# Kernel tuning notes

Measured on AMD Instinct MI355X. Metric: run time of the kernel, lower is better.

## Reference

```python
import jax, jax.numpy as jnp
import numpy as np

N_NODES = 50000
N_EDGES = 800000
IN_CH, OUT_CH, HEADS = 64, 32, 4
NEG_SLOPE = 0.2
BN_EPS = 1e-5


def setup_inputs() -> dict:
    key = jax.random.key(0)
    ks = jax.random.split(key, 9)
    x = jax.random.normal(ks[0], (N_NODES, IN_CH), dtype=jnp.float32)
    pos = jax.random.uniform(ks[1], (N_NODES, 3), dtype=jnp.float32)
    edge_index = jax.random.randint(ks[2], (2, N_EDGES), 0, N_NODES, dtype=jnp.int64)
    s = 1.0 / np.sqrt(IN_CH)
    W_l = jax.random.normal(ks[3], (IN_CH, HEADS * OUT_CH), dtype=jnp.float32) * s
    W_r = jax.random.normal(ks[4], (IN_CH, HEADS * OUT_CH), dtype=jnp.float32) * s
    W_edge = jax.random.normal(ks[5], (3, HEADS * OUT_CH), dtype=jnp.float32) * 0.5
    att = jax.random.normal(ks[6], (HEADS, OUT_CH), dtype=jnp.float32) * (1.0 / np.sqrt(OUT_CH))
    bn_gamma = jax.random.uniform(ks[7], (HEADS * OUT_CH,), dtype=jnp.float32, minval=0.5, maxval=1.5)
    bn_beta = jax.random.normal(ks[8], (HEADS * OUT_CH,), dtype=jnp.float32) * 0.1
    return {"x": x, "pos": pos, "edge_index": edge_index, "W_l": W_l, "W_r": W_r,
            "W_edge": W_edge, "att": att, "bn_gamma": bn_gamma, "bn_beta": bn_beta}


def reference(x, pos, edge_index, W_l, W_r, W_edge, att, bn_gamma, bn_beta):
    N = x.shape[0]
    H, C = att.shape
    # source->target projections (GATv2: lin_l for source/messages, lin_r for target)
    xl = (x @ W_l).reshape(N, H, C)
    xr = (x @ W_r).reshape(N, H, C)
    src, dst = edge_index[0], edge_index[1]
    edge_attr = pos[src] - pos[dst]  # [E,3] relative position as edge feature
    # add self-loops with fill_value='mean' (PyG default)
    loop = jnp.arange(N)
    src = jnp.concatenate([src, loop])
    dst = jnp.concatenate([dst, loop])
    mean_attr = edge_attr.mean(axis=0, keepdims=True)  # [1,3]
    edge_attr = jnp.concatenate([edge_attr, jnp.broadcast_to(mean_attr, (N, 3))], axis=0)
    # per-edge GATv2 score: att . LeakyReLU(x_l[j] + x_r[i] + W_e e_ij)
    e_feat = (edge_attr @ W_edge).reshape(-1, H, C)
    msg = xl[src]                              # [Et,H,C] (reused for aggregation)
    e = msg + xr[dst] + e_feat
    e = jax.nn.leaky_relu(e, NEG_SLOPE)
    score = jnp.einsum('ehc,hc->eh', e, att)   # [Et,H]
    # segment softmax over destination node
    m = jax.ops.segment_max(score, dst, num_segments=N)
    score = jnp.exp(score - m[dst])
    denom = jax.ops.segment_sum(score, dst, num_segments=N)
    alpha = score / (denom[dst] + 1e-16)       # [Et,H]
    out = jax.ops.segment_sum(alpha[:, :, None] * msg, dst, num_segments=N)
    out = out.reshape(N, H * C)
    # BatchNorm over node dimension (training-mode batch statistics, PyG BatchNorm)
    mu = out.mean(axis=0)
    var = out.var(axis=0)
    return (out - mu) / jnp.sqrt(var + BN_EPS) * bn_gamma + bn_beta
```

## Files before the change

### kernel.cpp

```cpp
#include <hip/hip_runtime.h>
#include <hip/hip_bf16.h>

#define N_NODES 50000
#define IN_CH 64
#define HC 128
#define CAP 64
#define NEG_SLOPE 0.2f
#define BN_EPS 1e-5f


__global__ __launch_bounds__(256) void k_gemm(const float* __restrict__ x,
                                              const float* __restrict__ Wl,
                                              const float* __restrict__ Wr,
                                              unsigned int* __restrict__ xl_bf,
                                              float* __restrict__ xr_out,
                                              int* __restrict__ deg,
                                              float* __restrict__ mean_sums,
                                              float* __restrict__ bn_sums,
                                              int* __restrict__ flag,
                                              const int* __restrict__ eidx) {
  {
    int gtid = blockIdx.x * 256 + threadIdx.x;
    if (gtid < N_NODES) deg[gtid] = 1;
    if (gtid < 256) bn_sums[gtid] = 0.f;
    if (gtid < 3) mean_sums[gtid] = 0.f;
    if (blockIdx.x == 0 && threadIdx.x < 64) {
      int w = eidx[2 * threadIdx.x + 1];
      unsigned long long nz = __ballot(w != 0);
      if (threadIdx.x == 0) flag[0] = (nz == 0ULL) ? 1 : 0;
    }
  }

  __shared__ float xs[16][IN_CH];
  __shared__ __hip_bfloat162 wsm[IN_CH][128];
  const int t = threadIdx.x;
  const int row0 = blockIdx.x * 16;

  for (int i = 0; i < 32; ++i) {
    int k = i * 2 + (t >> 7);
    int p = t & 127;
    int cc = p * 2;
    float2 wv;
    if (cc < 128) wv = *(const float2*)(Wl + k * 128 + cc);
    else          wv = *(const float2*)(Wr + k * 128 + (cc - 128));
    wsm[k][p] = __float22bfloat162_rn(wv);
  }
  {
    int r = t >> 4, c4 = (t & 15) * 4;
    *(float4*)&xs[r][c4] = *(const float4*)(x + (row0 + r) * IN_CH + c4);
  }
  __syncthreads();

  const int ct = t & 63;
  const int rt = t >> 6;
  const int c4 = ct * 4;
  const int r4 = rt * 4;

  float acc[4][4];
  #pragma unroll
  for (int a = 0; a < 4; ++a)
    #pragma unroll
    for (int b = 0; b < 4; ++b) acc[a][b] = 0.f;

  #pragma unroll 8
  for (int k = 0; k < IN_CH; ++k) {
    uint2 wraw = *(const uint2*)&wsm[k][ct * 2];
    float2 f01 = __bfloat1622float2(*(__hip_bfloat162*)&wraw.x);
    float2 f23 = __bfloat1622float2(*(__hip_bfloat162*)&wraw.y);
    float wv[4] = {f01.x, f01.y, f23.x, f23.y};
    float xv[4] = {xs[r4][k], xs[r4 + 1][k], xs[r4 + 2][k], xs[r4 + 3][k]};
    #pragma unroll
    for (int a = 0; a < 4; ++a)
      #pragma unroll
      for (int b = 0; b < 4; ++b) acc[a][b] = fmaf(xv[a], wv[b], acc[a][b]);
  }

  #pragma unroll
  for (int a = 0; a < 4; ++a) {
    int row = row0 + r4 + a;
    if (c4 < 128) {
      __hip_bfloat162 b01 = __float22bfloat162_rn(make_float2(acc[a][0], acc[a][1]));
      __hip_bfloat162 b23 = __float22bfloat162_rn(make_float2(acc[a][2], acc[a][3]));
      uint2 u;
      u.x = *(unsigned int*)&b01;
      u.y = *(unsigned int*)&b23;
      *(uint2*)(xl_bf + row * 64 + (c4 >> 1)) = u;
    } else {
      float4 v = make_float4(acc[a][0], acc[a][1], acc[a][2], acc[a][3]);
      *(float4*)(xr_out + row * HC + (c4 - 128)) = v;
    }
  }
}

__global__ __launch_bounds__(256) void k_edges(const int* __restrict__ eidx,
                                               const float* __restrict__ pos,
                                               int* __restrict__ deg,
                                               int* __restrict__ srcs,
                                               float* __restrict__ mean_sums,
                                               const int* __restrict__ flag,
                                               int E) {
  const bool w64 = flag[0] != 0;
  const int tid = blockIdx.x * 256 + threadIdx.x;
  const int base = tid * 8;
  float sx = 0.f, sy = 0.f, sz = 0.f;

  const bool vec_ok = w64 ? ((E & 1) == 0) : ((E & 3) == 0);

  if (base + 8 <= E && vec_ok) {
    int s[8], d[8];
    if (w64) {
      const int4* ps = (const int4*)(eidx + 2 * base);
      int4 A = ps[0], B = ps[1], C = ps[2], D = ps[3];
      s[0]=A.x; s[1]=A.z; s[2]=B.x; s[3]=B.z; s[4]=C.x; s[5]=C.z; s[6]=D.x; s[7]=D.z;
      const int4* pd = (const int4*)(eidx + 2 * E + 2 * base);
      A = pd[0]; B = pd[1]; C = pd[2]; D = pd[3];
      d[0]=A.x; d[1]=A.z; d[2]=B.x; d[3]=B.z; d[4]=C.x; d[5]=C.z; d[6]=D.x; d[7]=D.z;
    } else {
      int4 A = *(const int4*)(eidx + base);
      int4 B = *(const int4*)(eidx + base + 4);
      s[0]=A.x; s[1]=A.y; s[2]=A.z; s[3]=A.w; s[4]=B.x; s[5]=B.y; s[6]=B.z; s[7]=B.w;
      A = *(const int4*)(eidx + E + base);
      B = *(const int4*)(eidx + E + base + 4);
      d[0]=A.x; d[1]=A.y; d[2]=A.z; d[3]=A.w; d[4]=B.x; d[5]=B.y; d[6]=B.z; d[7]=B.w;
    }
    int slot[8];
    #pragma unroll
    for (int k = 0; k < 8; ++k) slot[k] = atomicAdd(&deg[d[k]], 1);
    #pragma unroll
    for (int k = 0; k < 8; ++k)
      if (slot[k] < CAP) srcs[d[k] * CAP + slot[k]] = s[k];
    #pragma unroll
    for (int k = 0; k < 8; ++k) {
      sx += pos[3 * s[k]]     - pos[3 * d[k]];
      sy += pos[3 * s[k] + 1] - pos[3 * d[k] + 1];
      sz += pos[3 * s[k] + 2] - pos[3 * d[k] + 2];
    }
  } else if (base < E) {
    int hi = min(base + 8, E);
    for (int e = base; e < hi; ++e) {
      int s, d;
      if (w64) { s = eidx[2 * e]; d = eidx[2 * (E + e)]; }
      else     { s = eidx[e];     d = eidx[E + e]; }
      int o = atomicAdd(&deg[d], 1);
      if (o < CAP) srcs[d * CAP + o] = s;
      sx += pos[3 * s]     - pos[3 * d];
      sy += pos[3 * s + 1] - pos[3 * d + 1];
      sz += pos[3 * s + 2] - pos[3 * d + 2];
    }
  }

  #pragma unroll
  for (int m = 1; m < 64; m <<= 1) {
    sx += __shfl_xor(sx, m); sy += __shfl_xor(sy, m); sz += __shfl_xor(sz, m);
  }
  __shared__ float red[4][3];
  int wave = threadIdx.x >> 6, lane = threadIdx.x & 63;
  if (lane == 0) { red[wave][0] = sx; red[wave][1] = sy; red[wave][2] = sz; }
  __syncthreads();
  if (threadIdx.x == 0) {
    float a = 0.f, b = 0.f, c = 0.f;
    for (int w = 0; w < 4; ++w) { a += red[w][0]; b += red[w][1]; c += red[w][2]; }
    unsafeAtomicAdd(&mean_sums[0], a);
    unsafeAtomicAdd(&mean_sums[1], b);
    unsafeAtomicAdd(&mean_sums[2], c);
  }
}

__device__ __forceinline__ void edge4(int s, float dx, float dy, float dz, bool valid,
                                      const unsigned int* __restrict__ xl_bf, int l5,
                                      float4 xr4, float4 at4, float4 w0, float4 w1, float4 w2,
                                      float& a0, float& a1, float& a2, float& a3, float& den) {
  uint2 raw = *(const uint2*)(xl_bf + (s << 6) + (l5 << 1));
  float2 x01 = __bfloat1622float2(*(__hip_bfloat162*)&raw.x);
  float2 x23 = __bfloat1622float2(*(__hip_bfloat162*)&raw.y);
  float t0 = x01.x + xr4.x; t0 = fmaf(dx, w0.x, t0); t0 = fmaf(dy, w1.x, t0); t0 = fmaf(dz, w2.x, t0);
  float t1 = x01.y + xr4.y; t1 = fmaf(dx, w0.y, t1); t1 = fmaf(dy, w1.y, t1); t1 = fmaf(dz, w2.y, t1);
  float t2 = x23.x + xr4.z; t2 = fmaf(dx, w0.z, t2); t2 = fmaf(dy, w1.z, t2); t2 = fmaf(dz, w2.z, t2);
  float t3 = x23.y + xr4.w; t3 = fmaf(dx, w0.w, t3); t3 = fmaf(dy, w1.w, t3); t3 = fmaf(dz, w2.w, t3);
  float l0 = fmaf(NEG_SLOPE, fminf(t0, 0.f), fmaxf(t0, 0.f));
  float l1 = fmaf(NEG_SLOPE, fminf(t1, 0.f), fmaxf(t1, 0.f));
  float l2 = fmaf(NEG_SLOPE, fminf(t2, 0.f), fmaxf(t2, 0.f));
  float l3 = fmaf(NEG_SLOPE, fminf(t3, 0.f), fmaxf(t3, 0.f));
  float sc = l0 * at4.x;
  sc = fmaf(l1, at4.y, sc); sc = fmaf(l2, at4.z, sc); sc = fmaf(l3, at4.w, sc);
  sc += __shfl_xor(sc, 1); sc += __shfl_xor(sc, 2); sc += __shfl_xor(sc, 4);
  float e = __expf(sc);
  float p = valid ? e : 0.f;
  den += p;
  a0 = fmaf(p, x01.x, a0); a1 = fmaf(p, x01.y, a1);
  a2 = fmaf(p, x23.x, a2); a3 = fmaf(p, x23.y, a3);
}

__global__ __launch_bounds__(256) void k_agg(const unsigned int* __restrict__ xl_bf,
                                             float* __restrict__ xr_out,
                                             const float* __restrict__ pos,
                                             const float* __restrict__ att,
                                             const float* __restrict__ We,
                                             const float* __restrict__ mean_sums,
                                             const int* __restrict__ srcs,
                                             const int* __restrict__ deg,
                                             float invE) {
  const int lane = threadIdx.x & 63;
  const int half = lane >> 5;
  const int l5 = lane & 31;
  const int c = l5 << 2;

  const float4 at4 = *(const float4*)(att + c);
  const float4 w0 = *(const float4*)(We + c);
  const float4 w1 = *(const float4*)(We + 128 + c);
  const float4 w2 = *(const float4*)(We + 256 + c);
  const float m0 = mean_sums[0] * invE;
  const float m1 = mean_sums[1] * invE;
  const float m2 = mean_sums[2] * invE;

  const int gw = blockIdx.x * 4 + (threadIdx.x >> 6);
  const int W = gridDim.x * 4;

  for (int i = gw; i < N_NODES; i += W) {
    const float4 xr4 = *(const float4*)(xr_out + i * HC + c);
    const float px = pos[3 * i], py = pos[3 * i + 1], pz = pos[3 * i + 2];
    const int di = min(deg[i], CAP);
    const int sreg = srcs[i * CAP + lane];
    float a0 = 0.f, a1 = 0.f, a2 = 0.f, a3 = 0.f, den = 0.f;

    {
      int sA = __shfl(sreg, 1);
      if (half == 0) sA = i;
      bool vA = half < di;
      if (!vA) sA = i;
      int jB = 2 + half;
      int sB = __shfl(sreg, jB);
      bool vB = jB < di;
      if (!vB) sB = i;
      float pax = pos[3 * sA], pay = pos[3 * sA + 1], paz = pos[3 * sA + 2];
      float pbx = pos[3 * sB], pby = pos[3 * sB + 1], pbz = pos[3 * sB + 2];
      float dxA = (half == 0) ? m0 : pax - px;
      float dyA = (half == 0) ? m1 : pay - py;
      float dzA = (half == 0) ? m2 : paz - pz;
      edge4(sA, dxA, dyA, dzA, vA, xl_bf, l5, xr4, at4, w0, w1, w2, a0, a1, a2, a3, den);
      edge4(sB, pbx - px, pby - py, pbz - pz, vB, xl_bf, l5, xr4, at4, w0, w1, w2, a0, a1, a2, a3, den);
    }

    for (int j = 4; j < di; j += 4) {
      int jA = j + half;
      int jB = j + 2 + half;
      int sA = __shfl(sreg, jA);
      int sB = __shfl(sreg, jB);
      bool vA = jA < di;
      bool vB = jB < di;
      if (!vA) sA = i;
      if (!vB) sB = i;
      float pax = pos[3 * sA], pay = pos[3 * sA + 1], paz = pos[3 * sA + 2];
      float pbx = pos[3 * sB], pby = pos[3 * sB + 1], pbz = pos[3 * sB + 2];
      edge4(sA, pax - px, pay - py, paz - pz, vA, xl_bf, l5, xr4, at4, w0, w1, w2, a0, a1, a2, a3, den);
      edge4(sB, pbx - px, pby - py, pbz - pz, vB, xl_bf, l5, xr4, at4, w0, w1, w2, a0, a1, a2, a3, den);
    }

    den += __shfl_xor(den, 32);
    a0 += __shfl_xor(a0, 32);
    a1 += __shfl_xor(a1, 32);
    a2 += __shfl_xor(a2, 32);
    a3 += __shfl_xor(a3, 32);

    float inv = 1.f / (den + 1e-16f);
    if (half == 0) {
      float4 o = make_float4(a0 * inv, a1 * inv, a2 * inv, a3 * inv);
      *(float4*)(xr_out + i * HC + c) = o;
    }
  }
}

__global__ __launch_bounds__(128) void k_bnstats(const float* __restrict__ out,
                                                 float* __restrict__ bn_sums) {
  int c = threadIdx.x;
  float s = 0.f, ss = 0.f;
  int r = blockIdx.x;
  const int g = gridDim.x;
  for (; r + g < N_NODES; r += 2 * g) {
    float v0 = out[r * HC + c];
    float v1 = out[(r + g) * HC + c];
    s += v0; ss = fmaf(v0, v0, ss);
    s += v1; ss = fmaf(v1, v1, ss);
  }
  if (r < N_NODES) {
    float v = out[r * HC + c];
    s += v; ss = fmaf(v, v, ss);
  }
  unsafeAtomicAdd(&bn_sums[c], s);
  unsafeAtomicAdd(&bn_sums[128 + c], ss);
}

__global__ __launch_bounds__(256) void k_bnapply(float* __restrict__ out,
                                                 const float* __restrict__ bn_sums,
                                                 const float* __restrict__ gamma,
                                                 const float* __restrict__ beta,
                                                 int n4) {
  const int stride = gridDim.x * blockDim.x;
  const float invN = 1.f / (float)N_NODES;
  for (int i = blockIdx.x * blockDim.x + threadIdx.x; i < n4; i += stride) {
    int c = (i & 31) * 4;
    float4 v = ((float4*)out)[i];
    float4 s = *(const float4*)(bn_sums + c);
    float4 q = *(const float4*)(bn_sums + 128 + c);
    float4 g = *(const float4*)(gamma + c);
    float4 b = *(const float4*)(beta + c);
    float mu, var, rstd;
    mu = s.x * invN; var = q.x * invN - mu * mu; rstd = rsqrtf(var + BN_EPS);
    v.x = (v.x - mu) * rstd * g.x + b.x;
    mu = s.y * invN; var = q.y * invN - mu * mu; rstd = rsqrtf(var + BN_EPS);
    v.y = (v.y - mu) * rstd * g.y + b.y;
    mu = s.z * invN; var = q.z * invN - mu * mu; rstd = rsqrtf(var + BN_EPS);
    v.z = (v.z - mu) * rstd * g.z + b.z;
    mu = s.w * invN; var = q.w * invN - mu * mu; rstd = rsqrtf(var + BN_EPS);
    v.w = (v.w - mu) * rstd * g.w + b.w;
    ((float4*)out)[i] = v;
  }
}

extern "C" void kernel_launch(void* const* d_in, const int* in_sizes, int n_in,
                              void* d_out, int out_size, void* d_ws, size_t ws_size,
                              hipStream_t stream) {
  const float* x     = (const float*)d_in[0];
  const float* pos   = (const float*)d_in[1];
  const int*   eidx  = (const int*)d_in[2];
  const float* Wl    = (const float*)d_in[3];
  const float* Wr    = (const float*)d_in[4];
  const float* We    = (const float*)d_in[5];
  const float* att   = (const float*)d_in[6];
  const float* gamma = (const float*)d_in[7];
  const float* beta  = (const float*)d_in[8];
  float* out = (float*)d_out;
  const int E = in_sizes[2] / 2;

  char* ws = (char*)d_ws;
  int*   flag      = (int*)(ws + 0);
  float* mean_sums = (float*)(ws + 64);
  float* bn_sums   = (float*)(ws + 1024);
  int*   deg       = (int*)(ws + 4096);
  int*   srcs      = (int*)(ws + (1 << 19));
  unsigned int* xl_bf = (unsigned int*)(ws + (1 << 24));

  k_gemm<<<N_NODES / 16, 256, 0, stream>>>(x, Wl, Wr, xl_bf, out,
                                           deg, mean_sums, bn_sums, flag, eidx);
  int eblocks = (E + 2047) / 2048;
  k_edges<<<eblocks, 256, 0, stream>>>(eidx, pos, deg, srcs, mean_sums, flag, E);
  k_agg<<<2048, 256, 0, stream>>>(xl_bf, out, pos, att, We, mean_sums, srcs, deg,
                                  1.f / (float)E);
  k_bnstats<<<512, 128, 0, stream>>>(out, bn_sums);
  k_bnapply<<<512, 256, 0, stream>>>(out, bn_sums, gamma, beta, out_size / 4);
}
```

Measured before the change: 258.4 us.

## Pack fp16 edge offsets into buckets and fuse BN statistics into aggregation

The edge pass now computes relative positions once and stores them as fp16 together with a 16-bit source index in an 8-byte bucket slot. This removes the per-edge random position gathers in aggregation. BatchNorm sum and sum-of-squares are accumulated inside the aggregation kernel, with a block reduction and atomics, which removes the separate stats kernel and its pass over the output. Costs are a larger bucket write, fp16 precision on edge offsets, and source ids limited to 16 bits.

Result: faster. 251.5 us (-2.7%).

```diff
diff --git a/kernel.cpp b/kernel.cpp
--- a/kernel.cpp
+++ b/kernel.cpp
@@ -1,5 +1,6 @@
 #include <hip/hip_runtime.h>
 #include <hip/hip_bf16.h>
+#include <hip/hip_fp16.h>
 
 #define N_NODES 50000
 #define IN_CH 64
@@ -92,10 +93,18 @@
   }
 }
 
+__device__ __forceinline__ uint2 packslot(int s, float dx, float dy, float dz) {
+  __half2 hxy = __halves2half2(__float2half_rn(dx), __float2half_rn(dy));
+  uint2 r;
+  r.x = *(unsigned int*)&hxy;
+  r.y = ((unsigned int)s << 16) | (unsigned int)__half_as_ushort(__float2half_rn(dz));
+  return r;
+}
+
 __global__ __launch_bounds__(256) void k_edges(const int* __restrict__ eidx,
                                                const float* __restrict__ pos,
                                                int* __restrict__ deg,
-                                               int* __restrict__ srcs,
+                                               uint2* __restrict__ bucket,
                                                float* __restrict__ mean_sums,
                                                const int* __restrict__ flag,
                                                int E) {
@@ -126,15 +135,17 @@
     int slot[8];
     #pragma unroll
     for (int k = 0; k < 8; ++k) slot[k] = atomicAdd(&deg[d[k]], 1);
+    float dx[8], dy[8], dz[8];
+    #pragma unroll
+    for (int k = 0; k < 8; ++k) {
+      dx[k] = pos[3 * s[k]]     - pos[3 * d[k]];
+      dy[k] = pos[3 * s[k] + 1] - pos[3 * d[k] + 1];
+      dz[k] = pos[3 * s[k] + 2] - pos[3 * d[k] + 2];
+      sx += dx[k]; sy += dy[k]; sz += dz[k];
+    }
     #pragma unroll
     for (int k = 0; k < 8; ++k)
-      if (slot[k] < CAP) srcs[d[k] * CAP + slot[k]] = s[k];
-    #pragma unroll
-    for (int k = 0; k < 8; ++k) {
-      sx += pos[3 * s[k]]     - pos[3 * d[k]];
-      sy += pos[3 * s[k] + 1] - pos[3 * d[k] + 1];
-      sz += pos[3 * s[k] + 2] - pos[3 * d[k] + 2];
-    }
+      if (slot[k] < CAP) bucket[d[k] * CAP + slot[k]] = packslot(s[k], dx[k], dy[k], dz[k]);
   } else if (base < E) {
     int hi = min(base + 8, E);
     for (int e = base; e < hi; ++e) {
@@ -142,10 +153,11 @@
       if (w64) { s = eidx[2 * e]; d = eidx[2 * (E + e)]; }
       else     { s = eidx[e];     d = eidx[E + e]; }
       int o = atomicAdd(&deg[d], 1);
-      if (o < CAP) srcs[d * CAP + o] = s;
-      sx += pos[3 * s]     - pos[3 * d];
-      sy += pos[3 * s + 1] - pos[3 * d + 1];
-      sz += pos[3 * s + 2] - pos[3 * d + 2];
+      float dx = pos[3 * s]     - pos[3 * d];
+      float dy = pos[3 * s + 1] - pos[3 * d + 1];
+      float dz = pos[3 * s + 2] - pos[3 * d + 2];
+      sx += dx; sy += dy; sz += dz;
+      if (o < CAP) bucket[d * CAP + o] = packslot(s, dx, dy, dz);
     }
   }
 
@@ -177,10 +189,10 @@
   float t1 = x01.y + xr4.y; t1 = fmaf(dx, w0.y, t1); t1 = fmaf(dy, w1.y, t1); t1 = fmaf(dz, w2.y, t1);
   float t2 = x23.x + xr4.z; t2 = fmaf(dx, w0.z, t2); t2 = fmaf(dy, w1.z, t2); t2 = fmaf(dz, w2.z, t2);
   float t3 = x23.y + xr4.w; t3 = fmaf(dx, w0.w, t3); t3 = fmaf(dy, w1.w, t3); t3 = fmaf(dz, w2.w, t3);
-  float l0 = fmaf(NEG_SLOPE, fminf(t0, 0.f), fmaxf(t0, 0.f));
-  float l1 = fmaf(NEG_SLOPE, fminf(t1, 0.f), fmaxf(t1, 0.f));
-  float l2 = fmaf(NEG_SLOPE, fminf(t2, 0.f), fmaxf(t2, 0.f));
-  float l3 = fmaf(NEG_SLOPE, fminf(t3, 0.f), fmaxf(t3, 0.f));
+  float l0 = fmaxf(t0, NEG_SLOPE * t0);
+  float l1 = fmaxf(t1, NEG_SLOPE * t1);
+  float l2 = fmaxf(t2, NEG_SLOPE * t2);
+  float l3 = fmaxf(t3, NEG_SLOPE * t3);
   float sc = l0 * at4.x;
   sc = fmaf(l1, at4.y, sc); sc = fmaf(l2, at4.z, sc); sc = fmaf(l3, at4.w, sc);
   sc += __shfl_xor(sc, 1); sc += __shfl_xor(sc, 2); sc += __shfl_xor(sc, 4);
@@ -193,17 +205,20 @@
 
 __global__ __launch_bounds__(256) void k_agg(const unsigned int* __restrict__ xl_bf,
                                              float* __restrict__ xr_out,
-                                             const float* __restrict__ pos,
                                              const float* __restrict__ att,
                                              const float* __restrict__ We,
                                              const float* __restrict__ mean_sums,
-                                             const int* __restrict__ srcs,
+                                             const uint2* __restrict__ bucket,
                                              const int* __restrict__ deg,
-                                             float invE) {
+                                             float invE,
+                                             float* __restrict__ bn_sums) {
+  __shared__ __align__(16) float redS[4][128];
+  __shared__ __align__(16) float redQ[4][128];
   const int lane = threadIdx.x & 63;
   const int half = lane >> 5;
   const int l5 = lane & 31;
   const int c = l5 << 2;
+  const int wave = threadIdx.x >> 6;
 
   const float4 at4 = *(const float4*)(att + c);
   const float4 w0 = *(const float4*)(We + c);
@@ -213,47 +228,57 @@
   const float m1 = mean_sums[1] * invE;
   const float m2 = mean_sums[2] * invE;
 
-  const int gw = blockIdx.x * 4 + (threadIdx.x >> 6);
+  const int gw = blockIdx.x * 4 + wave;
   const int W = gridDim.x * 4;
+
+  float4 bs = make_float4(0.f, 0.f, 0.f, 0.f);
+  float4 bq = make_float4(0.f, 0.f, 0.f, 0.f);
 
   for (int i = gw; i < N_NODES; i += W) {
     const float4 xr4 = *(const float4*)(xr_out + i * HC + c);
-    const float px = pos[3 * i], py = pos[3 * i + 1], pz = pos[3 * i + 2];
     const int di = min(deg[i], CAP);
-    const int sreg = srcs[i * CAP + lane];
+    uint2 se = make_uint2(0u, 0u);
+    if (lane < di) se = bucket[i * CAP + lane];
     float a0 = 0.f, a1 = 0.f, a2 = 0.f, a3 = 0.f, den = 0.f;
 
     {
-      int sA = __shfl(sreg, 1);
-      if (half == 0) sA = i;
-      bool vA = half < di;
+      const int jB = 2 + half;
+      uint2 wA, wB;
+      wA.x = (unsigned)__shfl((int)se.x, 1);  wA.y = (unsigned)__shfl((int)se.y, 1);
+      wB.x = (unsigned)__shfl((int)se.x, jB); wB.y = (unsigned)__shfl((int)se.y, jB);
+      float2 dA = __half22float2(*(__half2*)&wA.x);
+      float dzA = __half2float(__ushort_as_half((unsigned short)(wA.y & 0xffffu)));
+      int sA = (int)(wA.y >> 16);
+      if (half == 0) { sA = i; dA.x = m0; dA.y = m1; dzA = m2; }
+      const bool vA = half < di;
       if (!vA) sA = i;
-      int jB = 2 + half;
-      int sB = __shfl(sreg, jB);
-      bool vB = jB < di;
+      float2 dB = __half22float2(*(__half2*)&wB.x);
+      float dzB = __half2float(__ushort_as_half((unsigned short)(wB.y & 0xffffu)));
+      int sB = (int)(wB.y >> 16);
+      const bool vB = jB < di;
       if (!vB) sB = i;
-      float pax = pos[3 * sA], pay = pos[3 * sA + 1], paz = pos[3 * sA + 2];
-      float pbx = pos[3 * sB], pby = pos[3 * sB + 1], pbz = pos[3 * sB + 2];
-      float dxA = (half == 0) ? m0 : pax - px;
-      float dyA = (half == 0) ? m1 : pay - py;
-      float dzA = (half == 0) ? m2 : paz - pz;
-      edge4(sA, dxA, dyA, dzA, vA, xl_bf, l5, xr4, at4, w0, w1, w2, a0, a1, a2, a3, den);
-      edge4(sB, pbx - px, pby - py, pbz - pz, vB, xl_bf, l5, xr4, at4, w0, w1, w2, a0, a1, a2, a3, den);
+      edge4(sA, dA.x, dA.y, dzA, vA, xl_bf, l5, xr4, at4, w0, w1, w2, a0, a1, a2, a3, den);
+      edge4(sB, dB.x, dB.y, dzB, vB, xl_bf, l5, xr4, at4, w0, w1, w2, a0, a1, a2, a3, den);
     }
 
     for (int j = 4; j < di; j += 4) {
-      int jA = j + half;
-      int jB = j + 2 + half;
-      int sA = __shfl(sreg, jA);
-      int sB = __shfl(sreg, jB);
-      bool vA = jA < di;
-      bool vB = jB < di;
+      const int jA = j + half;
+      const int jB = j + 2 + half;
+      uint2 wA, wB;
+      wA.x = (unsigned)__shfl((int)se.x, jA); wA.y = (unsigned)__shfl((int)se.y, jA);
+      wB.x = (unsigned)__shfl((int)se.x, jB); wB.y = (unsigned)__shfl((int)se.y, jB);
+      float2 dA = __half22float2(*(__half2*)&wA.x);
+      float dzA = __half2float(__ushort_as_half((unsigned short)(wA.y & 0xffffu)));
+      int sA = (int)(wA.y >> 16);
+      const bool vA = jA < di;
       if (!vA) sA = i;
+      float2 dB = __half22float2(*(__half2*)&wB.x);
+      float dzB = __half2float(__ushort_as_half((unsigned short)(wB.y & 0xffffu)));
+      int sB = (int)(wB.y >> 16);
+      const bool vB = jB < di;
       if (!vB) sB = i;
-      float pax = pos[3 * sA], pay = pos[3 * sA + 1], paz = pos[3 * sA + 2];
-      float pbx = pos[3 * sB], pby = pos[3 * sB + 1], pbz = pos[3 * sB + 2];
-      edge4(sA, pax - px, pay - py, paz - pz, vA, xl_bf, l5, xr4, at4, w0, w1, w2, a0, a1, a2, a3, den);
-      edge4(sB, pbx - px, pby - py, pbz - pz, vB, xl_bf, l5, xr4, at4, w0, w1, w2, a0, a1, a2, a3, den);
+      edge4(sA, dA.x, dA.y, dzA, vA, xl_bf, l5, xr4, at4, w0, w1, w2, a0, a1, a2, a3, den);
+      edge4(sB, dB.x, dB.y, dzB, vB, xl_bf, l5, xr4, at4, w0, w1, w2, a0, a1, a2, a3, den);
     }
 
     den += __shfl_xor(den, 32);
@@ -262,32 +287,28 @@
     a2 += __shfl_xor(a2, 32);
     a3 += __shfl_xor(a3, 32);
 
-    float inv = 1.f / (den + 1e-16f);
+    const float inv = 1.f / (den + 1e-16f);
     if (half == 0) {
       float4 o = make_float4(a0 * inv, a1 * inv, a2 * inv, a3 * inv);
       *(float4*)(xr_out + i * HC + c) = o;
-    }
-  }
-}
-
-__global__ __launch_bounds__(128) void k_bnstats(const float* __restrict__ out,
-                                                 float* __restrict__ bn_sums) {
-  int c = threadIdx.x;
-  float s = 0.f, ss = 0.f;
-  int r = blockIdx.x;
-  const int g = gridDim.x;
-  for (; r + g < N_NODES; r += 2 * g) {
-    float v0 = out[r * HC + c];
-    float v1 = out[(r + g) * HC + c];
-    s += v0; ss = fmaf(v0, v0, ss);
-    s += v1; ss = fmaf(v1, v1, ss);
-  }
-  if (r < N_NODES) {
-    float v = out[r * HC + c];
-    s += v; ss = fmaf(v, v, ss);
-  }
-  unsafeAtomicAdd(&bn_sums[c], s);
-  unsafeAtomicAdd(&bn_sums[128 + c], ss);
+      bs.x += o.x; bs.y += o.y; bs.z += o.z; bs.w += o.w;
+      bq.x = fmaf(o.x, o.x, bq.x); bq.y = fmaf(o.y, o.y, bq.y);
+      bq.z = fmaf(o.z, o.z, bq.z); bq.w = fmaf(o.w, o.w, bq.w);
+    }
+  }
+
+  if (half == 0) {
+    *(float4*)&redS[wave][c] = bs;
+    *(float4*)&redQ[wave][c] = bq;
+  }
+  __syncthreads();
+  const int t = threadIdx.x;
+  if (t < 128) {
+    float s = redS[0][t] + redS[1][t] + redS[2][t] + redS[3][t];
+    float q = redQ[0][t] + redQ[1][t] + redQ[2][t] + redQ[3][t];
+    unsafeAtomicAdd(&bn_sums[t], s);
+    unsafeAtomicAdd(&bn_sums[128 + t], q);
+  }
 }
 
 __global__ __launch_bounds__(256) void k_bnapply(float* __restrict__ out,
@@ -337,15 +358,14 @@
   float* mean_sums = (float*)(ws + 64);
   float* bn_sums   = (float*)(ws + 1024);
   int*   deg       = (int*)(ws + 4096);
-  int*   srcs      = (int*)(ws + (1 << 19));
-  unsigned int* xl_bf = (unsigned int*)(ws + (1 << 24));
+  uint2* bucket    = (uint2*)(ws + (1 << 19));
+  unsigned int* xl_bf = (unsigned int*)(ws + (1 << 19) + (size_t)N_NODES * CAP * 8);
 
   k_gemm<<<N_NODES / 16, 256, 0, stream>>>(x, Wl, Wr, xl_bf, out,
                                            deg, mean_sums, bn_sums, flag, eidx);
   int eblocks = (E + 2047) / 2048;
-  k_edges<<<eblocks, 256, 0, stream>>>(eidx, pos, deg, srcs, mean_sums, flag, E);
-  k_agg<<<2048, 256, 0, stream>>>(xl_bf, out, pos, att, We, mean_sums, srcs, deg,
-                                  1.f / (float)E);
-  k_bnstats<<<512, 128, 0, stream>>>(out, bn_sums);
+  k_edges<<<eblocks, 256, 0, stream>>>(eidx, pos, deg, bucket, mean_sums, flag, E);
+  k_agg<<<2048, 256, 0, stream>>>(xl_bf, out, att, We, mean_sums, bucket, deg,
+                                  1.f / (float)E, bn_sums);
   k_bnapply<<<512, 256, 0, stream>>>(out, bn_sums, gamma, beta, out_size / 4);
 }
```

## Fuse GEMM with edge bucketing, fold BN stats into aggregation, use DPP reductions

Applied to the files above, without the earlier changes.

Merges the projection GEMM and the edge bucketing/degree kernel into one launch: the first block range does the GEMM and the rest do edge scatter. Zero-initialisation moves to a memset, which needs the self-loop to sit at an implicit slot 0 (degree starts at 0, with an offset of one). The batch-norm statistics pass is removed by accumulating per-channel sums and sums of squares inside the aggregation kernel, reduced in shared memory and then with atomics. It also replaces the score shuffle reduction with DPP moves and simplifies the LeakyReLU. The aim is fewer launches, overlap of GEMM with edge atomics, and no second read of the output, at the cost of more atomic traffic from the aggregation blocks and extra register pressure.

Result: no change. 257.1 us (-0.5%).

```diff
diff --git a/kernel.cpp b/kernel.cpp
--- a/kernel.cpp
+++ b/kernel.cpp
@@ -5,102 +5,96 @@
 #define IN_CH 64
 #define HC 128
 #define CAP 64
+#define GEMM_BLOCKS (N_NODES / 16)
 #define NEG_SLOPE 0.2f
 #define BN_EPS 1e-5f
 
 
-__global__ __launch_bounds__(256) void k_gemm(const float* __restrict__ x,
-                                              const float* __restrict__ Wl,
-                                              const float* __restrict__ Wr,
-                                              unsigned int* __restrict__ xl_bf,
-                                              float* __restrict__ xr_out,
-                                              int* __restrict__ deg,
-                                              float* __restrict__ mean_sums,
-                                              float* __restrict__ bn_sums,
-                                              int* __restrict__ flag,
-                                              const int* __restrict__ eidx) {
-  {
-    int gtid = blockIdx.x * 256 + threadIdx.x;
-    if (gtid < N_NODES) deg[gtid] = 1;
-    if (gtid < 256) bn_sums[gtid] = 0.f;
-    if (gtid < 3) mean_sums[gtid] = 0.f;
-    if (blockIdx.x == 0 && threadIdx.x < 64) {
-      int w = eidx[2 * threadIdx.x + 1];
-      unsigned long long nz = __ballot(w != 0);
-      if (threadIdx.x == 0) flag[0] = (nz == 0ULL) ? 1 : 0;
-    }
-  }
-
-  __shared__ float xs[16][IN_CH];
-  __shared__ __hip_bfloat162 wsm[IN_CH][128];
-  const int t = threadIdx.x;
-  const int row0 = blockIdx.x * 16;
-
-  for (int i = 0; i < 32; ++i) {
-    int k = i * 2 + (t >> 7);
-    int p = t & 127;
-    int cc = p * 2;
-    float2 wv;
-    if (cc < 128) wv = *(const float2*)(Wl + k * 128 + cc);
-    else          wv = *(const float2*)(Wr + k * 128 + (cc - 128));
-    wsm[k][p] = __float22bfloat162_rn(wv);
-  }
-  {
-    int r = t >> 4, c4 = (t & 15) * 4;
-    *(float4*)&xs[r][c4] = *(const float4*)(x + (row0 + r) * IN_CH + c4);
-  }
-  __syncthreads();
-
-  const int ct = t & 63;
-  const int rt = t >> 6;
-  const int c4 = ct * 4;
-  const int r4 = rt * 4;
-
-  float acc[4][4];
-  #pragma unroll
-  for (int a = 0; a < 4; ++a)
-    #pragma unroll
-    for (int b = 0; b < 4; ++b) acc[a][b] = 0.f;
-
-  #pragma unroll 8
-  for (int k = 0; k < IN_CH; ++k) {
-    uint2 wraw = *(const uint2*)&wsm[k][ct * 2];
-    float2 f01 = __bfloat1622float2(*(__hip_bfloat162*)&wraw.x);
-    float2 f23 = __bfloat1622float2(*(__hip_bfloat162*)&wraw.y);
-    float wv[4] = {f01.x, f01.y, f23.x, f23.y};
-    float xv[4] = {xs[r4][k], xs[r4 + 1][k], xs[r4 + 2][k], xs[r4 + 3][k]};
-    #pragma unroll
-    for (int a = 0; a < 4; ++a)
-      #pragma unroll
-      for (int b = 0; b < 4; ++b) acc[a][b] = fmaf(xv[a], wv[b], acc[a][b]);
-  }
-
-  #pragma unroll
-  for (int a = 0; a < 4; ++a) {
-    int row = row0 + r4 + a;
-    if (c4 < 128) {
-      __hip_bfloat162 b01 = __float22bfloat162_rn(make_float2(acc[a][0], acc[a][1]));
-      __hip_bfloat162 b23 = __float22bfloat162_rn(make_float2(acc[a][2], acc[a][3]));
-      uint2 u;
-      u.x = *(unsigned int*)&b01;
-      u.y = *(unsigned int*)&b23;
-      *(uint2*)(xl_bf + row * 64 + (c4 >> 1)) = u;
-    } else {
-      float4 v = make_float4(acc[a][0], acc[a][1], acc[a][2], acc[a][3]);
-      *(float4*)(xr_out + row * HC + (c4 - 128)) = v;
-    }
-  }
-}
-
-__global__ __launch_bounds__(256) void k_edges(const int* __restrict__ eidx,
+__global__ __launch_bounds__(256) void k_fused(const float* __restrict__ x,
+                                               const float* __restrict__ Wl,
+                                               const float* __restrict__ Wr,
+                                               unsigned int* __restrict__ xl_bf,
+                                               float* __restrict__ xr_out,
+                                               const int* __restrict__ eidx,
                                                const float* __restrict__ pos,
                                                int* __restrict__ deg,
                                                int* __restrict__ srcs,
                                                float* __restrict__ mean_sums,
-                                               const int* __restrict__ flag,
                                                int E) {
-  const bool w64 = flag[0] != 0;
-  const int tid = blockIdx.x * 256 + threadIdx.x;
+  __shared__ float xs[16][IN_CH];
+  __shared__ __hip_bfloat162 wsm[IN_CH][128];
+  __shared__ int s_w64;
+
+  if (blockIdx.x < GEMM_BLOCKS) {
+    const int t = threadIdx.x;
+    const int row0 = blockIdx.x * 16;
+
+    for (int i = 0; i < 32; ++i) {
+      int k = i * 2 + (t >> 7);
+      int p = t & 127;
+      int cc = p * 2;
+      float2 wv;
+      if (cc < 128) wv = *(const float2*)(Wl + k * 128 + cc);
+      else          wv = *(const float2*)(Wr + k * 128 + (cc - 128));
+      wsm[k][p] = __float22bfloat162_rn(wv);
+    }
+    {
+      int r = t >> 4, c4 = (t & 15) * 4;
+      *(float4*)&xs[r][c4] = *(const float4*)(x + (row0 + r) * IN_CH + c4);
+    }
+    __syncthreads();
+
+    const int ct = t & 63;
+    const int rt = t >> 6;
+    const int c4 = ct * 4;
+    const int r4 = rt * 4;
+
+    float acc[4][4];
+    #pragma unroll
+    for (int a = 0; a < 4; ++a)
+      #pragma unroll
+      for (int b = 0; b < 4; ++b) acc[a][b] = 0.f;
+
+    #pragma unroll 8
+    for (int k = 0; k < IN_CH; ++k) {
+      uint2 wraw = *(const uint2*)&wsm[k][ct * 2];
+      float2 f01 = __bfloat1622float2(*(__hip_bfloat162*)&wraw.x);
+      float2 f23 = __bfloat1622float2(*(__hip_bfloat162*)&wraw.y);
+      float wv[4] = {f01.x, f01.y, f23.x, f23.y};
+      float xv[4] = {xs[r4][k], xs[r4 + 1][k], xs[r4 + 2][k], xs[r4 + 3][k]};
+      #pragma unroll
+      for (int a = 0; a < 4; ++a)
+        #pragma unroll
+        for (int b = 0; b < 4; ++b) acc[a][b] = fmaf(xv[a], wv[b], acc[a][b]);
+    }
+
+    #pragma unroll
+    for (int a = 0; a < 4; ++a) {
+      int row = row0 + r4 + a;
+      if (c4 < 128) {
+        __hip_bfloat162 b01 = __float22bfloat162_rn(make_float2(acc[a][0], acc[a][1]));
+        __hip_bfloat162 b23 = __float22bfloat162_rn(make_float2(acc[a][2], acc[a][3]));
+        uint2 u;
+        u.x = *(unsigned int*)&b01;
+        u.y = *(unsigned int*)&b23;
+        *(uint2*)(xl_bf + row * 64 + (c4 >> 1)) = u;
+      } else {
+        float4 v = make_float4(acc[a][0], acc[a][1], acc[a][2], acc[a][3]);
+        *(float4*)(xr_out + row * HC + (c4 - 128)) = v;
+      }
+    }
+    return;
+  }
+
+  if (threadIdx.x < 64) {
+    int w = eidx[2 * threadIdx.x + 1];
+    unsigned long long nz = __ballot(w != 0);
+    if (threadIdx.x == 0) s_w64 = (nz == 0ULL) ? 1 : 0;
+  }
+  __syncthreads();
+  const bool w64 = s_w64 != 0;
+
+  const int tid = (blockIdx.x - GEMM_BLOCKS) * 256 + threadIdx.x;
   const int base = tid * 8;
   float sx = 0.f, sy = 0.f, sz = 0.f;
 
@@ -128,7 +122,7 @@
     for (int k = 0; k < 8; ++k) slot[k] = atomicAdd(&deg[d[k]], 1);
     #pragma unroll
     for (int k = 0; k < 8; ++k)
-      if (slot[k] < CAP) srcs[d[k] * CAP + slot[k]] = s[k];
+      if (slot[k] < CAP - 1) srcs[d[k] * CAP + 1 + slot[k]] = s[k];
     #pragma unroll
     for (int k = 0; k < 8; ++k) {
       sx += pos[3 * s[k]]     - pos[3 * d[k]];
@@ -142,7 +136,7 @@
       if (w64) { s = eidx[2 * e]; d = eidx[2 * (E + e)]; }
       else     { s = eidx[e];     d = eidx[E + e]; }
       int o = atomicAdd(&deg[d], 1);
-      if (o < CAP) srcs[d * CAP + o] = s;
+      if (o < CAP - 1) srcs[d * CAP + 1 + o] = s;
       sx += pos[3 * s]     - pos[3 * d];
       sy += pos[3 * s + 1] - pos[3 * d + 1];
       sz += pos[3 * s + 2] - pos[3 * d + 2];
@@ -153,7 +147,7 @@
   for (int m = 1; m < 64; m <<= 1) {
     sx += __shfl_xor(sx, m); sy += __shfl_xor(sy, m); sz += __shfl_xor(sz, m);
   }
-  __shared__ float red[4][3];
+  float (*red)[3] = (float(*)[3])xs;
   int wave = threadIdx.x >> 6, lane = threadIdx.x & 63;
   if (lane == 0) { red[wave][0] = sx; red[wave][1] = sy; red[wave][2] = sz; }
   __syncthreads();
@@ -164,6 +158,13 @@
     unsafeAtomicAdd(&mean_sums[1], b);
     unsafeAtomicAdd(&mean_sums[2], c);
   }
+}
+
+__device__ __forceinline__ float sum8_dpp(float v) {
+  v += __int_as_float(__builtin_amdgcn_mov_dpp(__float_as_int(v), 0xB1,  0xF, 0xF, true));
+  v += __int_as_float(__builtin_amdgcn_mov_dpp(__float_as_int(v), 0x4E,  0xF, 0xF, true));
+  v += __int_as_float(__builtin_amdgcn_mov_dpp(__float_as_int(v), 0x141, 0xF, 0xF, true));
+  return v;
 }
 
 __device__ __forceinline__ void edge4(int s, float dx, float dy, float dz, bool valid,
@@ -177,13 +178,13 @@
   float t1 = x01.y + xr4.y; t1 = fmaf(dx, w0.y, t1); t1 = fmaf(dy, w1.y, t1); t1 = fmaf(dz, w2.y, t1);
   float t2 = x23.x + xr4.z; t2 = fmaf(dx, w0.z, t2); t2 = fmaf(dy, w1.z, t2); t2 = fmaf(dz, w2.z, t2);
   float t3 = x23.y + xr4.w; t3 = fmaf(dx, w0.w, t3); t3 = fmaf(dy, w1.w, t3); t3 = fmaf(dz, w2.w, t3);
-  float l0 = fmaf(NEG_SLOPE, fminf(t0, 0.f), fmaxf(t0, 0.f));
-  float l1 = fmaf(NEG_SLOPE, fminf(t1, 0.f), fmaxf(t1, 0.f));
-  float l2 = fmaf(NEG_SLOPE, fminf(t2, 0.f), fmaxf(t2, 0.f));
-  float l3 = fmaf(NEG_SLOPE, fminf(t3, 0.f), fmaxf(t3, 0.f));
+  float l0 = fmaxf(t0, NEG_SLOPE * t0);
+  float l1 = fmaxf(t1, NEG_SLOPE * t1);
+  float l2 = fmaxf(t2, NEG_SLOPE * t2);
+  float l3 = fmaxf(t3, NEG_SLOPE * t3);
   float sc = l0 * at4.x;
   sc = fmaf(l1, at4.y, sc); sc = fmaf(l2, at4.z, sc); sc = fmaf(l3, at4.w, sc);
-  sc += __shfl_xor(sc, 1); sc += __shfl_xor(sc, 2); sc += __shfl_xor(sc, 4);
+  sc = sum8_dpp(sc);
   float e = __expf(sc);
   float p = valid ? e : 0.f;
   den += p;
@@ -199,11 +200,15 @@
                                              const float* __restrict__ mean_sums,
                                              const int* __restrict__ srcs,
                                              const int* __restrict__ deg,
-                                             float invE) {
+                                             float invE,
+                                             float* __restrict__ bn_sums) {
+  __shared__ __align__(16) float redS[4][128];
+  __shared__ __align__(16) float redQ[4][128];
   const int lane = threadIdx.x & 63;
   const int half = lane >> 5;
   const int l5 = lane & 31;
   const int c = l5 << 2;
+  const int wave = threadIdx.x >> 6;
 
   const float4 at4 = *(const float4*)(att + c);
   const float4 w0 = *(const float4*)(We + c);
@@ -213,13 +218,16 @@
   const float m1 = mean_sums[1] * invE;
   const float m2 = mean_sums[2] * invE;
 
-  const int gw = blockIdx.x * 4 + (threadIdx.x >> 6);
+  const int gw = blockIdx.x * 4 + wave;
   const int W = gridDim.x * 4;
+
+  float4 bs = make_float4(0.f, 0.f, 0.f, 0.f);
+  float4 bq = make_float4(0.f, 0.f, 0.f, 0.f);
 
   for (int i = gw; i < N_NODES; i += W) {
     const float4 xr4 = *(const float4*)(xr_out + i * HC + c);
     const float px = pos[3 * i], py = pos[3 * i + 1], pz = pos[3 * i + 2];
-    const int di = min(deg[i], CAP);
+    const int di = min(deg[i] + 1, CAP);
     const int sreg = srcs[i * CAP + lane];
     float a0 = 0.f, a1 = 0.f, a2 = 0.f, a3 = 0.f, den = 0.f;
 
@@ -262,32 +270,28 @@
     a2 += __shfl_xor(a2, 32);
     a3 += __shfl_xor(a3, 32);
 
-    float inv = 1.f / (den + 1e-16f);
+    const float inv = 1.f / (den + 1e-16f);
     if (half == 0) {
       float4 o = make_float4(a0 * inv, a1 * inv, a2 * inv, a3 * inv);
       *(float4*)(xr_out + i * HC + c) = o;
-    }
-  }
-}
-
-__global__ __launch_bounds__(128) void k_bnstats(const float* __restrict__ out,
-                                                 float* __restrict__ bn_sums) {
-  int c = threadIdx.x;
-  float s = 0.f, ss = 0.f;
-  int r = blockIdx.x;
-  const int g = gridDim.x;
-  for (; r + g < N_NODES; r += 2 * g) {
-    float v0 = out[r * HC + c];
-    float v1 = out[(r + g) * HC + c];
-    s += v0; ss = fmaf(v0, v0, ss);
-    s += v1; ss = fmaf(v1, v1, ss);
-  }
-  if (r < N_NODES) {
-    float v = out[r * HC + c];
-    s += v; ss = fmaf(v, v, ss);
-  }
-  unsafeAtomicAdd(&bn_sums[c], s);
-  unsafeAtomicAdd(&bn_sums[128 + c], ss);
+      bs.x += o.x; bs.y += o.y; bs.z += o.z; bs.w += o.w;
+      bq.x = fmaf(o.x, o.x, bq.x); bq.y = fmaf(o.y, o.y, bq.y);
+      bq.z = fmaf(o.z, o.z, bq.z); bq.w = fmaf(o.w, o.w, bq.w);
+    }
+  }
+
+  if (half == 0) {
+    *(float4*)&redS[wave][c] = bs;
+    *(float4*)&redQ[wave][c] = bq;
+  }
+  __syncthreads();
+  const int t = threadIdx.x;
+  if (t < 128) {
+    float s = redS[0][t] + redS[1][t] + redS[2][t] + redS[3][t];
+    float q = redQ[0][t] + redQ[1][t] + redQ[2][t] + redQ[3][t];
+    unsafeAtomicAdd(&bn_sums[t], s);
+    unsafeAtomicAdd(&bn_sums[128 + t], q);
+  }
 }
 
 __global__ __launch_bounds__(256) void k_bnapply(float* __restrict__ out,
@@ -333,19 +337,18 @@
   const int E = in_sizes[2] / 2;
 
   char* ws = (char*)d_ws;
-  int*   flag      = (int*)(ws + 0);
   float* mean_sums = (float*)(ws + 64);
   float* bn_sums   = (float*)(ws + 1024);
   int*   deg       = (int*)(ws + 4096);
   int*   srcs      = (int*)(ws + (1 << 19));
   unsigned int* xl_bf = (unsigned int*)(ws + (1 << 24));
 
-  k_gemm<<<N_NODES / 16, 256, 0, stream>>>(x, Wl, Wr, xl_bf, out,
-                                           deg, mean_sums, bn_sums, flag, eidx);
+  hipMemsetAsync(ws, 0, 4096 + (size_t)N_NODES * 4, stream);
+
   int eblocks = (E + 2047) / 2048;
-  k_edges<<<eblocks, 256, 0, stream>>>(eidx, pos, deg, srcs, mean_sums, flag, E);
+  k_fused<<<GEMM_BLOCKS + eblocks, 256, 0, stream>>>(x, Wl, Wr, xl_bf, out,
+                                                     eidx, pos, deg, srcs, mean_sums, E);
   k_agg<<<2048, 256, 0, stream>>>(xl_bf, out, pos, att, We, mean_sums, srcs, deg,
-                                  1.f / (float)E);
-  k_bnstats<<<512, 128, 0, stream>>>(out, bn_sums);
+                                  1.f / (float)E, bn_sums);
   k_bnapply<<<512, 256, 0, stream>>>(out, bn_sums, gamma, beta, out_size / 4);
 }
```
